# Optimization experiments

Hardware: AMD Instinct MI355X
Metric: run time of the kernel (lower is better)

Reference implementation:

```python
import math
import jax, jax.numpy as jnp
import numpy as np

VOCAB, EMB, ADIM, HEADS = 32000, 512, 64, 8
B, S = 8, 1024
SIGMOID_DOMAIN = 5.0
LN_EPS = 1e-5


def setup_inputs() -> dict:
    key = jax.random.key(0)
    k = jax.random.split(key, 7)
    x = jax.random.randint(k[0], (B, S), 0, VOCAB, dtype=jnp.int64 if jax.config.read('jax_enable_x64') else jnp.int32)
    emb_table = jax.random.normal(k[1], (VOCAB, EMB), dtype=jnp.float32)
    gamma = jnp.ones((EMB,), dtype=jnp.float32)
    beta = jnp.zeros((EMB,), dtype=jnp.float32)
    # torch.rand -> uniform [0, 1)
    Wq = jax.random.uniform(k[2], (HEADS, ADIM, EMB), dtype=jnp.float32)
    Wk = jax.random.uniform(k[3], (HEADS, ADIM, EMB), dtype=jnp.float32)
    Wv = jax.random.uniform(k[4], (HEADS, EMB, EMB), dtype=jnp.float32)
    return {"x": x, "emb_table": emb_table, "gamma": gamma, "beta": beta,
            "Wq": Wq, "Wk": Wk, "Wv": Wv}


def reference(x, emb_table, gamma, beta, Wq, Wk, Wv):
    # Embedding + LayerNorm -> [B, S, E]
    e = emb_table[x]
    mu = jnp.mean(e, axis=-1, keepdims=True)
    var = jnp.mean((e - mu) ** 2, axis=-1, keepdims=True)
    h = (e - mu) / jnp.sqrt(var + LN_EPS) * gamma + beta

    # per-head projections: W [H, A, E] x h [B, S, E] -> [B, H, S, A]
    q = jnp.einsum('hae,bse->bhsa', Wq, h)
    k = jnp.einsum('hae,bse->bhsa', Wk, h)
    v = jnp.einsum('hve,bse->bhsv', Wv, h)  # v_dim == E

    scale = math.sqrt(EMB)
    scores = jnp.einsum('bhsa,bhta->bhst', q, k) / scale  # [B, H, S, S]

    # overtaking-sigmoid: per-row min-max normalize, blend softmax with sigmoid
    s_max = jnp.max(scores, axis=-1, keepdims=True)
    s_min = jnp.min(scores, axis=-1, keepdims=True)
    sn = (scores - s_min) / (s_max - s_min)
    softmax_sel = 1.0 - jnp.max(sn, axis=-1, keepdims=True)
    sigmoid_sel = 1.0 - softmax_sel
    weights = (softmax_sel * jax.nn.softmax(sn, axis=-1)
               + sigmoid_sel * jax.nn.sigmoid(sn * (2.0 * SIGMOID_DOMAIN) - SIGMOID_DOMAIN))

    out = jnp.einsum('bhst,bhtv->bhsv', weights, v)  # [B, H, S, E]
    return out
```

## Files before the change

kernel.cpp:

```cpp
#include <hip/hip_runtime.h>
#include <math.h>

#define NB 8
#define NH 8
#define NS 1024
#define NE 512
#define NA 64
#define NBH (NB*NH)

typedef short s8v __attribute__((ext_vector_type(8)));
typedef float f4v __attribute__((ext_vector_type(4)));
typedef unsigned short u4v __attribute__((ext_vector_type(4)));

#define MFMA16(a,b,c) __builtin_amdgcn_mfma_f32_16x16x32_bf16((a),(b),(c),0,0,0)

static __device__ __forceinline__ unsigned short f2bf(float f) {
    union { float f; unsigned u; } c; c.f = f;
    unsigned r = c.u + 0x7FFF + ((c.u >> 16) & 1);
    return (unsigned short)(r >> 16);
}
static __device__ __forceinline__ s8v ld8(const unsigned short* p) {
    return *(const s8v*)p;
}
static __device__ __forceinline__ void gload16(const unsigned short* g, unsigned short* l) {
    __builtin_amdgcn_global_load_lds(
        (const __attribute__((address_space(1))) unsigned char*)g,
        (__attribute__((address_space(3))) unsigned char*)l, 16, 0, 0);
}

static __device__ __forceinline__ void stage_tile(
    const unsigned short* src, size_t stride, int k0,
    unsigned short* lds, int tid)
{
    int w = tid >> 6, l = tid & 63;
    #pragma unroll
    for (int c = 0; c < 4; ++c) {
        int chunk = w * 4 + c;
        int row = chunk * 8 + (l >> 3);
        gload16(src + (size_t)row * stride + k0 + (l & 7) * 8,
                lds + chunk * 512 + l * 8);
    }
}

static __device__ __forceinline__ void stage_tile_sw(
    const unsigned short* src, size_t stride,
    unsigned short* lds, int tid)
{
    int w = tid >> 6, l = tid & 63;
    #pragma unroll
    for (int c = 0; c < 4; ++c) {
        int chunk = w * 4 + c;
        int row = chunk * 8 + (l >> 3);
        gload16(src + (size_t)row * stride + (((l & 7) ^ (row & 7)) * 8),
                lds + chunk * 512 + l * 8);
    }
}

__global__ __launch_bounds__(256) void k_embed_ln(
    const int* __restrict__ x, const float* __restrict__ emb,
    const float* __restrict__ gamma, const float* __restrict__ beta,
    unsigned short* __restrict__ hb)
{
    int row = blockIdx.x;
    int tok = x[row];
    const float* e = emb + (size_t)tok * NE;
    int t = threadIdx.x;
    float v0 = e[t], v1 = e[t + 256];
    float sum = v0 + v1, ssq = v0 * v0 + v1 * v1;
    #pragma unroll
    for (int o = 32; o > 0; o >>= 1) {
        sum += __shfl_xor(sum, o);
        ssq += __shfl_xor(ssq, o);
    }
    __shared__ float wsum[4], wssq[4];
    __shared__ float mu_s, rstd_s;
    int wid = t >> 6;
    if ((t & 63) == 0) { wsum[wid] = sum; wssq[wid] = ssq; }
    __syncthreads();
    if (t == 0) {
        float S1 = wsum[0] + wsum[1] + wsum[2] + wsum[3];
        float S2 = wssq[0] + wssq[1] + wssq[2] + wssq[3];
        float mu = S1 / NE;
        float var = S2 / NE - mu * mu;
        mu_s = mu;
        rstd_s = rsqrtf(var + 1e-5f);
    }
    __syncthreads();
    float mu = mu_s, rstd = rstd_s;
    unsigned short* hr = hb + (size_t)row * NE;
    hr[t]       = f2bf((v0 - mu) * rstd * gamma[t]       + beta[t]);
    hr[t + 256] = f2bf((v1 - mu) * rstd * gamma[t + 256] + beta[t + 256]);
}

__global__ __launch_bounds__(256) void k_cvt3(
    const float* __restrict__ Wq, const float* __restrict__ Wk,
    const float* __restrict__ Wv,
    unsigned short* __restrict__ wqb, unsigned short* __restrict__ wkb,
    unsigned short* __restrict__ wvb, int nqk, int nv)
{
    int i = blockIdx.x * 256 + threadIdx.x;
    if (i < nqk)            wqb[i] = f2bf(Wq[i]);
    else if (i < 2 * nqk)   wkb[i - nqk] = f2bf(Wk[i - nqk]);
    else if (i < 2 * nqk + nv) wvb[i - 2 * nqk] = f2bf(Wv[i - 2 * nqk]);
}

__global__ __launch_bounds__(256) void k_qk_gemm(
    const unsigned short* __restrict__ hb, const unsigned short* __restrict__ wqb,
    const unsigned short* __restrict__ wkb,
    unsigned short* __restrict__ qb, unsigned short* __restrict__ kbf)
{
    int bid = blockIdx.x;
    int b2 = (bid & 7) * 64 + (bid >> 3);
    int st = b2 & 7, bh = b2 >> 3;
    int b = bh >> 3, hh = bh & 7;
    int tid = threadIdx.x;
    int w = tid >> 6, l = tid & 63;
    int lo = l & 15, hi = l >> 4;
    int wr = w >> 1, wc = w & 1;

    __shared__ __align__(16) unsigned short As[128 * 64];
    __shared__ __align__(16) unsigned short Bs[128 * 64];

    f4v acc[4][4];
    f4v z = {0.f, 0.f, 0.f, 0.f};
    #pragma unroll
    for (int i = 0; i < 4; ++i)
        #pragma unroll
        for (int j = 0; j < 4; ++j) acc[i][j] = z;

    const unsigned short* asrc = hb + ((size_t)(b * NS) + st * 128) * NE;
    for (int kt = 0; kt < 8; ++kt) {
        int k0 = kt * 64;
        stage_tile(asrc, NE, k0, As, tid);
        {
            #pragma unroll
            for (int c = 0; c < 4; ++c) {
                int chunk = w * 4 + c;
                int row = chunk * 8 + (l >> 3);
                const unsigned short* bsrc = (chunk < 8)
                    ? wqb + ((size_t)(hh * NA) + row) * NE
                    : wkb + ((size_t)(hh * NA) + row - 64) * NE;
                gload16(bsrc + k0 + (l & 7) * 8, Bs + chunk * 512 + l * 8);
            }
        }
        __syncthreads();
        #pragma unroll
        for (int ks = 0; ks < 2; ++ks) {
            s8v af[4], bf[4];
            #pragma unroll
            for (int sub = 0; sub < 4; ++sub)
                af[sub] = ld8(As + (wr * 64 + sub * 16 + lo) * 64 + ks * 32 + hi * 8);
            #pragma unroll
            for (int es = 0; es < 4; ++es)
                bf[es] = ld8(Bs + (wc * 64 + es * 16 + lo) * 64 + ks * 32 + hi * 8);
            #pragma unroll
            for (int sub = 0; sub < 4; ++sub)
                #pragma unroll
                for (int es = 0; es < 4; ++es)
                    acc[sub][es] = MFMA16(af[sub], bf[es], acc[sub][es]);
        }
        __syncthreads();
    }
    unsigned short* dst = (wc == 0) ? qb : kbf;
    #pragma unroll
    for (int sub = 0; sub < 4; ++sub)
        #pragma unroll
        for (int es = 0; es < 4; ++es)
            #pragma unroll
            for (int i = 0; i < 4; ++i) {
                int s = st * 128 + wr * 64 + sub * 16 + hi * 4 + i;
                int a = es * 16 + lo;
                dst[((size_t)bh * NS + s) * NA + a] = f2bf(acc[sub][es][i]);
            }
}

__global__ __launch_bounds__(256) void k_v_gemm(
    const unsigned short* __restrict__ hb, const unsigned short* __restrict__ wvb,
    unsigned short* __restrict__ vtb)
{
    int bid = blockIdx.x;
    int b2 = (bid & 7) * 256 + (bid >> 3);
    int tt = b2 & 7;
    int et = (b2 >> 3) & 3;
    int bh = b2 >> 5;
    int b = bh >> 3, hh = bh & 7;
    int tid = threadIdx.x;
    int w = tid >> 6, l = tid & 63;
    int lo = l & 15, hi = l >> 4;
    int wr = w >> 1, wc = w & 1;

    __shared__ __align__(16) unsigned short As[128 * 64];
    __shared__ __align__(16) unsigned short Bs[128 * 64];

    f4v acc[4][4];
    f4v z = {0.f, 0.f, 0.f, 0.f};
    #pragma unroll
    for (int i = 0; i < 4; ++i)
        #pragma unroll
        for (int j = 0; j < 4; ++j) acc[i][j] = z;

    const unsigned short* asrc = wvb + ((size_t)(hh * NE) + et * 128) * NE;
    const unsigned short* bsrc = hb + ((size_t)(b * NS) + tt * 128) * NE;
    for (int kt = 0; kt < 8; ++kt) {
        int k0 = kt * 64;
        stage_tile(asrc, NE, k0, As, tid);
        stage_tile(bsrc, NE, k0, Bs, tid);
        __syncthreads();
        #pragma unroll
        for (int ks = 0; ks < 2; ++ks) {
            s8v af[4], bf[4];
            #pragma unroll
            for (int sub = 0; sub < 4; ++sub)
                af[sub] = ld8(As + (wr * 64 + sub * 16 + lo) * 64 + ks * 32 + hi * 8);
            #pragma unroll
            for (int es = 0; es < 4; ++es)
                bf[es] = ld8(Bs + (wc * 64 + es * 16 + lo) * 64 + ks * 32 + hi * 8);
            #pragma unroll
            for (int sub = 0; sub < 4; ++sub)
                #pragma unroll
                for (int es = 0; es < 4; ++es)
                    acc[sub][es] = MFMA16(af[sub], bf[es], acc[sub][es]);
        }
        __syncthreads();
    }
    #pragma unroll
    for (int sub = 0; sub < 4; ++sub)
        #pragma unroll
        for (int es = 0; es < 4; ++es)
            #pragma unroll
            for (int i = 0; i < 4; ++i) {
                int e_ = et * 128 + wr * 64 + sub * 16 + hi * 4 + i;
                int t_ = tt * 128 + wc * 64 + es * 16 + lo;
                vtb[((size_t)bh * NE + e_) * NS + t_] = f2bf(acc[sub][es][i]);
            }
}

__global__ __launch_bounds__(256) void k_minmax_mfma(
    const unsigned short* __restrict__ qb, const unsigned short* __restrict__ kbf,
    float* __restrict__ rmn, float* __restrict__ rmx)
{
    int bid = blockIdx.x;
    int b2 = (bid & 7) * 128 + (bid >> 3);
    int qt = b2 & 15, bh = b2 >> 4;
    int tid = threadIdx.x;
    int w = tid >> 6, l = tid & 63;
    int lo = l & 15, hi = l >> 4;
    int s0 = qt * 64 + w * 16;

    const unsigned short* qp = qb + ((size_t)bh * NS + s0 + lo) * NA + hi * 8;
    s8v a0 = ld8(qp), a1 = ld8(qp + 32);

    __shared__ __align__(16) unsigned short Ks[128 * 64];

    float mn = 1e30f, mx = -1e30f;
    const unsigned short* ksrc = kbf + (size_t)bh * NS * NA;
    for (int t0 = 0; t0 < NS; t0 += 128) {
        __syncthreads();
        stage_tile_sw(ksrc + (size_t)t0 * NA, NA, Ks, tid);
        __syncthreads();
        #pragma unroll
        for (int tf = 0; tf < 8; ++tf) {
            int r = tf * 16 + lo;
            s8v b0 = ld8(Ks + r * 64 + ((hi ^ (lo & 7)) * 8));
            s8v b1 = ld8(Ks + r * 64 + (((hi + 4) ^ (lo & 7)) * 8));
            f4v c = {0.f, 0.f, 0.f, 0.f};
            c = MFMA16(b0, a0, c);
            c = MFMA16(b1, a1, c);
            mn = fminf(mn, fminf(fminf(c[0], c[1]), fminf(c[2], c[3])));
            mx = fmaxf(mx, fmaxf(fmaxf(c[0], c[1]), fmaxf(c[2], c[3])));
        }
    }
    mn = fminf(mn, __shfl_xor(mn, 16));
    mn = fminf(mn, __shfl_xor(mn, 32));
    mx = fmaxf(mx, __shfl_xor(mx, 16));
    mx = fmaxf(mx, __shfl_xor(mx, 32));
    if (l < 16) {
        rmn[(size_t)bh * NS + s0 + l] = mn;
        rmx[(size_t)bh * NS + s0 + l] = mx;
    }
}

#define WSTR 136
__global__ __launch_bounds__(512, 2) void k_attn_fused(
    const unsigned short* __restrict__ qb, const unsigned short* __restrict__ kbf,
    const unsigned short* __restrict__ vtb, const float* __restrict__ rmn,
    const float* __restrict__ rmx, float* __restrict__ out)
{
    int bid = blockIdx.x;
    int b2 = (bid & 7) * 64 + (bid >> 3);
    int qt = b2 & 7, bh = b2 >> 3;
    int s0 = qt * 128;
    int tid = threadIdx.x;
    int w = tid >> 6, l = tid & 63;
    int lo = l & 15, hi = l >> 4;

    __shared__ __align__(16) unsigned short Qs[128 * 64];
    __shared__ __align__(16) unsigned short wt[2][128 * WSTR];

    #pragma unroll
    for (int j = 0; j < 2; ++j) {
        int ch = j * 512 + tid;
        int row = ch >> 3, cc = ch & 7;
        s8v qv = ld8(qb + ((size_t)bh * NS + s0 + row) * NA + cc * 8);
        *(s8v*)(Qs + row * 64 + ((cc ^ (row & 7)) * 8)) = qv;
    }

    float invv[8], n2v[8];
    #pragma unroll
    for (int sub = 0; sub < 8; ++sub) {
        int r = s0 + sub * 16 + lo;
        float mn = rmn[(size_t)bh * NS + r];
        float iv = __builtin_amdgcn_rcpf(rmx[(size_t)bh * NS + r] - mn);
        invv[sub] = iv;
        n2v[sub] = -mn * iv;
    }

    const unsigned short* kframe = kbf + (size_t)bh * NS * NA;
    const unsigned short* vbase = vtb + ((size_t)bh * NE + w * 64) * NS;

    f4v acc[8][4];
    f4v z = {0.f, 0.f, 0.f, 0.f};
    #pragma unroll
    for (int sub = 0; sub < 8; ++sub)
        #pragma unroll
        for (int es = 0; es < 4; ++es) acc[sub][es] = z;

    auto loadK = [&](int t0, s8v& k0, s8v& k1) {
        const unsigned short* kp = kframe + (size_t)(t0 + w * 16 + lo) * NA + hi * 8;
        k0 = ld8(kp);
        k1 = ld8(kp + 32);
    };

    auto scores = [&](s8v k0, s8v k1, unsigned short* wbuf) {
        #pragma unroll
        for (int sub = 0; sub < 8; ++sub) {
            int r = sub * 16 + lo;
            s8v q0 = ld8(Qs + r * 64 + ((hi ^ (lo & 7)) * 8));
            s8v q1 = ld8(Qs + r * 64 + (((hi + 4) ^ (lo & 7)) * 8));
            f4v c = z;
            c = MFMA16(k0, q0, c);
            c = MFMA16(k1, q1, c);
            u4v pk;
            #pragma unroll
            for (int i = 0; i < 4; ++i) {
                float sn = fmaf(c[i], invv[sub], n2v[sub]);
                float arg = fmaf(sn, -14.4269504089f, 7.2134752044f);
                float e = __builtin_amdgcn_exp2f(arg);
                pk[i] = f2bf(__builtin_amdgcn_rcpf(1.f + e));
            }
            *(u4v*)(wbuf + (sub * 16 + lo) * WSTR + w * 16 + hi * 4) = pk;
        }
    };

    s8v kc0, kc1, kn0, kn1;
    loadK(0, kc0, kc1);
    __syncthreads();
    scores(kc0, kc1, wt[0]);
    for (int it = 0; it < 8; ++it) {
        int t0 = it * 128;
        if (it < 7) loadK(t0 + 128, kn0, kn1);
        asm volatile("s_waitcnt lgkmcnt(0)" ::: "memory");
        __builtin_amdgcn_s_barrier();
        __builtin_amdgcn_sched_barrier(0);
        {
            const unsigned short* wb = wt[it & 1];
            #pragma unroll
            for (int ks = 0; ks < 4; ++ks) {
                s8v bv[4];
                #pragma unroll
                for (int es = 0; es < 4; ++es)
                    bv[es] = ld8(vbase + (size_t)(es * 16 + lo) * NS + t0 + ks * 32 + hi * 8);
                #pragma unroll
                for (int sub = 0; sub < 8; ++sub) {
                    s8v aw = ld8(wb + (sub * 16 + lo) * WSTR + ks * 32 + hi * 8);
                    #pragma unroll
                    for (int es = 0; es < 4; ++es)
                        acc[sub][es] = MFMA16(aw, bv[es], acc[sub][es]);
                }
            }
        }
        if (it < 7) scores(kn0, kn1, wt[(it + 1) & 1]);
    }
    #pragma unroll
    for (int sub = 0; sub < 8; ++sub)
        #pragma unroll
        for (int es = 0; es < 4; ++es)
            #pragma unroll
            for (int i = 0; i < 4; ++i)
                out[((size_t)bh * NS + s0 + sub * 16 + hi * 4 + i) * NE
                    + w * 64 + es * 16 + lo] = acc[sub][es][i];
}

extern "C" void kernel_launch(void* const* d_in, const int* in_sizes, int n_in,
                              void* d_out, int out_size, void* d_ws, size_t ws_size,
                              hipStream_t stream) {
    const int*   x     = (const int*)d_in[0];
    const float* emb   = (const float*)d_in[1];
    const float* gamma = (const float*)d_in[2];
    const float* beta  = (const float*)d_in[3];
    const float* Wq    = (const float*)d_in[4];
    const float* Wk    = (const float*)d_in[5];
    const float* Wv    = (const float*)d_in[6];
    float* out = (float*)d_out;

    unsigned short* p = (unsigned short*)d_ws;
    unsigned short* hb  = p;  p += (size_t)NB * NS * NE;
    unsigned short* qb  = p;  p += (size_t)NBH * NS * NA;
    unsigned short* kb  = p;  p += (size_t)NBH * NS * NA;
    unsigned short* vtb = p;  p += (size_t)NBH * NS * NE;
    unsigned short* wqb = p;  p += (size_t)NH * NA * NE;
    unsigned short* wkb = p;  p += (size_t)NH * NA * NE;
    unsigned short* wvb = p;  p += (size_t)NH * NE * NE;
    float* rmn = (float*)p;
    float* rmx = rmn + (size_t)NBH * NS;

    const int nqk = NH * NA * NE, nv = NH * NE * NE;
    k_cvt3<<<(2 * nqk + nv + 255) / 256, 256, 0, stream>>>(Wq, Wk, Wv, wqb, wkb, wvb, nqk, nv);
    k_embed_ln<<<NB * NS, 256, 0, stream>>>(x, emb, gamma, beta, hb);
    k_qk_gemm<<<512, 256, 0, stream>>>(hb, wqb, wkb, qb, kb);
    k_v_gemm<<<2048, 256, 0, stream>>>(hb, wvb, vtb);
    k_minmax_mfma<<<1024, 256, 0, stream>>>(qb, kb, rmn, rmx);
    k_attn_fused<<<512, 512, 0, stream>>>(qb, kb, vtb, rmn, rmx, out);
}
```

Baseline: 225.3 us.

## Fuse row min/max pass into attention kernel and drop separate minmax launch

The separate k_minmax_mfma kernel is removed. k_attn_fused now first computes QK^T over all keys with Q held in LDS, reduces per-row min/max across waves through shared memory, and then runs the normalize-and-PV pass. This removes one kernel launch and the global round trip of the min/max arrays. The cost is that each attention block computes QK twice and uses extra LDS, which may reduce occupancy.

```diff
diff --git a/kernel.cpp b/kernel.cpp
--- a/kernel.cpp
+++ b/kernel.cpp
@@ -38,20 +38,6 @@
         int chunk = w * 4 + c;
         int row = chunk * 8 + (l >> 3);
         gload16(src + (size_t)row * stride + k0 + (l & 7) * 8,
-                lds + chunk * 512 + l * 8);
-    }
-}
-
-static __device__ __forceinline__ void stage_tile_sw(
-    const unsigned short* src, size_t stride,
-    unsigned short* lds, int tid)
-{
-    int w = tid >> 6, l = tid & 63;
-    #pragma unroll
-    for (int c = 0; c < 4; ++c) {
-        int chunk = w * 4 + c;
-        int row = chunk * 8 + (l >> 3);
-        gload16(src + (size_t)row * stride + (((l & 7) ^ (row & 7)) * 8),
                 lds + chunk * 512 + l * 8);
     }
 }
@@ -235,56 +221,10 @@
             }
 }
 
-__global__ __launch_bounds__(256) void k_minmax_mfma(
-    const unsigned short* __restrict__ qb, const unsigned short* __restrict__ kbf,
-    float* __restrict__ rmn, float* __restrict__ rmx)
-{
-    int bid = blockIdx.x;
-    int b2 = (bid & 7) * 128 + (bid >> 3);
-    int qt = b2 & 15, bh = b2 >> 4;
-    int tid = threadIdx.x;
-    int w = tid >> 6, l = tid & 63;
-    int lo = l & 15, hi = l >> 4;
-    int s0 = qt * 64 + w * 16;
-
-    const unsigned short* qp = qb + ((size_t)bh * NS + s0 + lo) * NA + hi * 8;
-    s8v a0 = ld8(qp), a1 = ld8(qp + 32);
-
-    __shared__ __align__(16) unsigned short Ks[128 * 64];
-
-    float mn = 1e30f, mx = -1e30f;
-    const unsigned short* ksrc = kbf + (size_t)bh * NS * NA;
-    for (int t0 = 0; t0 < NS; t0 += 128) {
-        __syncthreads();
-        stage_tile_sw(ksrc + (size_t)t0 * NA, NA, Ks, tid);
-        __syncthreads();
-        #pragma unroll
-        for (int tf = 0; tf < 8; ++tf) {
-            int r = tf * 16 + lo;
-            s8v b0 = ld8(Ks + r * 64 + ((hi ^ (lo & 7)) * 8));
-            s8v b1 = ld8(Ks + r * 64 + (((hi + 4) ^ (lo & 7)) * 8));
-            f4v c = {0.f, 0.f, 0.f, 0.f};
-            c = MFMA16(b0, a0, c);
-            c = MFMA16(b1, a1, c);
-            mn = fminf(mn, fminf(fminf(c[0], c[1]), fminf(c[2], c[3])));
-            mx = fmaxf(mx, fmaxf(fmaxf(c[0], c[1]), fmaxf(c[2], c[3])));
-        }
-    }
-    mn = fminf(mn, __shfl_xor(mn, 16));
-    mn = fminf(mn, __shfl_xor(mn, 32));
-    mx = fmaxf(mx, __shfl_xor(mx, 16));
-    mx = fmaxf(mx, __shfl_xor(mx, 32));
-    if (l < 16) {
-        rmn[(size_t)bh * NS + s0 + l] = mn;
-        rmx[(size_t)bh * NS + s0 + l] = mx;
-    }
-}
-
 #define WSTR 136
 __global__ __launch_bounds__(512, 2) void k_attn_fused(
     const unsigned short* __restrict__ qb, const unsigned short* __restrict__ kbf,
-    const unsigned short* __restrict__ vtb, const float* __restrict__ rmn,
-    const float* __restrict__ rmx, float* __restrict__ out)
+    const unsigned short* __restrict__ vtb, float* __restrict__ out)
 {
     int bid = blockIdx.x;
     int b2 = (bid & 7) * 64 + (bid >> 3);
@@ -296,6 +236,7 @@
 
     __shared__ __align__(16) unsigned short Qs[128 * 64];
     __shared__ __align__(16) unsigned short wt[2][128 * WSTR];
+    __shared__ float pmn[8][128], pmx[8][128];
 
     #pragma unroll
     for (int j = 0; j < 2; ++j) {
@@ -305,38 +246,83 @@
         *(s8v*)(Qs + row * 64 + ((cc ^ (row & 7)) * 8)) = qv;
     }
 
-    float invv[8], n2v[8];
-    #pragma unroll
-    for (int sub = 0; sub < 8; ++sub) {
-        int r = s0 + sub * 16 + lo;
-        float mn = rmn[(size_t)bh * NS + r];
-        float iv = __builtin_amdgcn_rcpf(rmx[(size_t)bh * NS + r] - mn);
-        invv[sub] = iv;
-        n2v[sub] = -mn * iv;
-    }
-
     const unsigned short* kframe = kbf + (size_t)bh * NS * NA;
     const unsigned short* vbase = vtb + ((size_t)bh * NE + w * 64) * NS;
-
-    f4v acc[8][4];
-    f4v z = {0.f, 0.f, 0.f, 0.f};
-    #pragma unroll
-    for (int sub = 0; sub < 8; ++sub)
-        #pragma unroll
-        for (int es = 0; es < 4; ++es) acc[sub][es] = z;
 
     auto loadK = [&](int t0, s8v& k0, s8v& k1) {
         const unsigned short* kp = kframe + (size_t)(t0 + w * 16 + lo) * NA + hi * 8;
         k0 = ld8(kp);
         k1 = ld8(kp + 32);
     };
+    auto loadQ = [&](int sub, s8v& q0, s8v& q1) {
+        int r = sub * 16 + lo;
+        q0 = ld8(Qs + r * 64 + ((hi ^ (lo & 7)) * 8));
+        q1 = ld8(Qs + r * 64 + (((hi + 4) ^ (lo & 7)) * 8));
+    };
+
+    f4v z = {0.f, 0.f, 0.f, 0.f};
+    s8v kc0, kc1, kn0, kn1;
+
+    __syncthreads();
+    float mnp[8], mxp[8];
+    #pragma unroll
+    for (int sub = 0; sub < 8; ++sub) { mnp[sub] = 1e30f; mxp[sub] = -1e30f; }
+    loadK(0, kc0, kc1);
+    for (int it = 0; it < 8; ++it) {
+        if (it < 7) loadK((it + 1) * 128, kn0, kn1);
+        #pragma unroll
+        for (int sub = 0; sub < 8; ++sub) {
+            s8v q0, q1;
+            loadQ(sub, q0, q1);
+            f4v c = z;
+            c = MFMA16(kc0, q0, c);
+            c = MFMA16(kc1, q1, c);
+            mnp[sub] = fminf(mnp[sub], fminf(fminf(c[0], c[1]), fminf(c[2], c[3])));
+            mxp[sub] = fmaxf(mxp[sub], fmaxf(fmaxf(c[0], c[1]), fmaxf(c[2], c[3])));
+        }
+        kc0 = kn0; kc1 = kn1;
+    }
+    #pragma unroll
+    for (int sub = 0; sub < 8; ++sub) {
+        mnp[sub] = fminf(mnp[sub], __shfl_xor(mnp[sub], 16));
+        mnp[sub] = fminf(mnp[sub], __shfl_xor(mnp[sub], 32));
+        mxp[sub] = fmaxf(mxp[sub], __shfl_xor(mxp[sub], 16));
+        mxp[sub] = fmaxf(mxp[sub], __shfl_xor(mxp[sub], 32));
+    }
+    if (l < 16) {
+        #pragma unroll
+        for (int sub = 0; sub < 8; ++sub) {
+            pmn[w][sub * 16 + l] = mnp[sub];
+            pmx[w][sub * 16 + l] = mxp[sub];
+        }
+    }
+    __syncthreads();
+    float invv[8], n2v[8];
+    #pragma unroll
+    for (int sub = 0; sub < 8; ++sub) {
+        int q = sub * 16 + lo;
+        float mn = pmn[0][q], mx = pmx[0][q];
+        #pragma unroll
+        for (int j = 1; j < 8; ++j) {
+            mn = fminf(mn, pmn[j][q]);
+            mx = fmaxf(mx, pmx[j][q]);
+        }
+        float iv = __builtin_amdgcn_rcpf(mx - mn);
+        invv[sub] = iv;
+        n2v[sub] = -mn * iv;
+    }
+
+    f4v acc[8][4];
+    #pragma unroll
+    for (int sub = 0; sub < 8; ++sub)
+        #pragma unroll
+        for (int es = 0; es < 4; ++es) acc[sub][es] = z;
 
     auto scores = [&](s8v k0, s8v k1, unsigned short* wbuf) {
         #pragma unroll
         for (int sub = 0; sub < 8; ++sub) {
-            int r = sub * 16 + lo;
-            s8v q0 = ld8(Qs + r * 64 + ((hi ^ (lo & 7)) * 8));
-            s8v q1 = ld8(Qs + r * 64 + (((hi + 4) ^ (lo & 7)) * 8));
+            s8v q0, q1;
+            loadQ(sub, q0, q1);
             f4v c = z;
             c = MFMA16(k0, q0, c);
             c = MFMA16(k1, q1, c);
@@ -352,9 +338,7 @@
         }
     };
 
-    s8v kc0, kc1, kn0, kn1;
     loadK(0, kc0, kc1);
-    __syncthreads();
     scores(kc0, kc1, wt[0]);
     for (int it = 0; it < 8; ++it) {
         int t0 = it * 128;
@@ -411,14 +395,11 @@
     unsigned short* wqb = p;  p += (size_t)NH * NA * NE;
     unsigned short* wkb = p;  p += (size_t)NH * NA * NE;
     unsigned short* wvb = p;  p += (size_t)NH * NE * NE;
-    float* rmn = (float*)p;
-    float* rmx = rmn + (size_t)NBH * NS;
 
     const int nqk = NH * NA * NE, nv = NH * NE * NE;
     k_cvt3<<<(2 * nqk + nv + 255) / 256, 256, 0, stream>>>(Wq, Wk, Wv, wqb, wkb, wvb, nqk, nv);
     k_embed_ln<<<NB * NS, 256, 0, stream>>>(x, emb, gamma, beta, hb);
     k_qk_gemm<<<512, 256, 0, stream>>>(hb, wqb, wkb, qb, kb);
     k_v_gemm<<<2048, 256, 0, stream>>>(hb, wvb, vtb);
-    k_minmax_mfma<<<1024, 256, 0, stream>>>(qb, kb, rmn, rmx);
-    k_attn_fused<<<512, 512, 0, stream>>>(qb, kb, vtb, rmn, rmx, out);
-}
+    k_attn_fused<<<512, 512, 0, stream>>>(qb, kb, vtb, out);
+}
```

New measurement: 214.8 us. 1.05x faster.
